# Kernel optimization log

Measured on AMD Instinct MI355X. Metric: run time of the kernel, lower is better.

The kernel has to match this reference:

```python
import jax, jax.numpy as jnp
import numpy as np

T = 1024          # tokens (flattened batch*seq)
H = 1024          # hidden_size
NH = 8            # num_attention_heads
NKV = 4           # num_key_value_heads
HD = H // NH      # head_dim = 128
E = 32            # n_routed_experts
TOPK = 4          # num_experts_per_tok
NG = 8            # n_group
TKG = 4           # topk_group
MI = 512          # moe_intermediate_size
SI = MI * 2       # shared experts intermediate (n_shared_experts=2)
THETA = 10000.0
EPS = 1e-6
RSF = 2.5         # routed_scaling_factor


def setup_inputs() -> dict:
    key = jax.random.key(0)
    ks = jax.random.split(key, 16)
    s = jnp.float32(0.02)
    def nrm(k, shape):
        return jax.random.normal(k, shape, jnp.float32) * s
    return {
        "hidden_states": jax.random.normal(ks[0], (T, H), jnp.float32),
        "position_ids": jnp.arange(T, dtype=jnp.int32),
        "ln1_w": jnp.ones((H,), jnp.float32),
        "ln2_w": jnp.ones((H,), jnp.float32),
        "q_w": nrm(ks[1], (H, H)),            # torch Linear layout [out, in]
        "k_w": nrm(ks[2], (NKV * HD, H)),
        "v_w": nrm(ks[3], (NKV * HD, H)),
        "o_w": nrm(ks[4], (H, H)),
        "router_w": nrm(ks[5], (E, H)),
        "router_bias": jnp.zeros((E,), jnp.float32),  # e_score_correction_bias
        "eg_w": nrm(ks[6], (E, H, MI)),       # expert gate_proj, [E, in, out]
        "eu_w": nrm(ks[7], (E, H, MI)),       # expert up_proj
        "ed_w": nrm(ks[8], (E, MI, H)),       # expert down_proj
        "sg_w": nrm(ks[9], (H, SI)),          # shared experts gate_proj, [in, out]
        "su_w": nrm(ks[10], (H, SI)),
        "sd_w": nrm(ks[11], (SI, H)),
    }


def rmsnorm(x, w):
    var = jnp.mean(x * x, axis=-1, keepdims=True)
    return x * jax.lax.rsqrt(var + EPS) * w


def apply_rope(x, pos):
    # x: [T, heads, HD], non-interleaved (half-rotation)
    half = HD // 2
    inv_freq = 1.0 / (THETA ** (jnp.arange(half, dtype=jnp.float32) / half))
    freqs = pos.astype(jnp.float32)[:, None] * inv_freq[None, :]  # [T, half]
    cos = jnp.cos(freqs)[:, None, :]
    sin = jnp.sin(freqs)[:, None, :]
    x1, x2 = x[..., :half], x[..., half:]
    return jnp.concatenate([x1 * cos - x2 * sin, x2 * cos + x1 * sin], axis=-1)


def attention(h, pos, q_w, k_w, v_w, o_w):
    q = (h @ q_w.T).reshape(T, NH, HD)
    k = (h @ k_w.T).reshape(T, NKV, HD)
    v = (h @ v_w.T).reshape(T, NKV, HD)
    q = apply_rope(q, pos)
    k = apply_rope(k, pos)
    rep = NH // NKV
    k = jnp.repeat(k, rep, axis=1)  # [T, NH, HD]
    v = jnp.repeat(v, rep, axis=1)
    scale = 1.0 / np.sqrt(HD).astype(np.float32)
    scores = jnp.einsum("qhd,khd->hqk", q, k) * scale  # [NH, T, T]
    causal = jnp.tril(jnp.ones((T, T), bool))
    scores = jnp.where(causal[None], scores, jnp.finfo(scores.dtype).min)
    probs = jax.nn.softmax(scores, axis=-1)
    out = jnp.einsum("hqk,khd->qhd", probs, v).reshape(T, H)
    return out @ o_w.T


def router(x, router_w, router_bias):
    logits = x.astype(jnp.float32) @ router_w.T  # [T, E]
    scores = jax.nn.sigmoid(logits)
    sfc = scores + router_bias[None, :]
    # group-limited routing: sum of top-2 per group
    group_scores = jax.lax.top_k(sfc.reshape(T, NG, E // NG), 2)[0].sum(-1)  # [T, NG]
    gidx = jax.lax.top_k(group_scores, TKG)[1]  # [T, TKG]
    gmask = jnp.zeros((T, NG), jnp.float32).at[jnp.arange(T)[:, None], gidx].set(1.0)
    smask = jnp.repeat(gmask, E // NG, axis=1) > 0  # [T, E]
    masked = jnp.where(smask, sfc, 0.0)
    topk_idx = jax.lax.top_k(masked, TOPK)[1]  # [T, TOPK]
    topk_w = jnp.take_along_axis(scores, topk_idx, axis=1)
    topk_w = topk_w / (topk_w.sum(-1, keepdims=True) + 1e-20)  # norm_topk_prob
    return topk_idx, topk_w * RSF


def moe(x, router_w, router_bias, eg_w, eu_w, ed_w, sg_w, su_w, sd_w):
    topk_idx, topk_w = router(x, router_w, router_bias)
    # combine weights [T, E]
    cw = jnp.zeros((T, E), jnp.float32).at[jnp.arange(T)[:, None], topk_idx].add(topk_w)
    g = jnp.einsum("th,ehi->eti", x, eg_w)
    u = jnp.einsum("th,ehi->eti", x, eu_w)
    a = jax.nn.silu(g) * u
    o = jnp.einsum("eti,eih->eth", a, ed_w)
    routed = jnp.einsum("eth,te->th", o, cw)
    shared = (jax.nn.silu(x @ sg_w) * (x @ su_w)) @ sd_w
    return routed + shared


def reference(hidden_states, position_ids, ln1_w, ln2_w, q_w, k_w, v_w, o_w,
              router_w, router_bias, eg_w, eu_w, ed_w, sg_w, su_w, sd_w):
    res = hidden_states
    h = rmsnorm(hidden_states, ln1_w)
    h = attention(h, position_ids, q_w, k_w, v_w, o_w)
    h = res + h
    res = h
    h = rmsnorm(h, ln2_w)
    h = moe(h, router_w, router_bias, eg_w, eu_w, ed_w, sg_w, su_w, sd_w)
    return h + res
```

## Files before the change

kernel.cpp:

```cpp
#include <hip/hip_runtime.h>
#include <math.h>

#define T 1024
#define H 1024
#define NH 8
#define NKV 4
#define HD 128
#define NE 32
#define TOPK 4
#define NG 8
#define MI 512
#define SI 1024
#define RSF 2.5f
#define EPS 1e-6f

#define ASPLIT 4
#define SPLITK 256

typedef short bf16x8 __attribute__((ext_vector_type(8)));
typedef float f32x4 __attribute__((ext_vector_type(4)));
#define MFMA16(a, b, c) __builtin_amdgcn_mfma_f32_16x16x32_bf16((a), (b), (c), 0, 0, 0)

__device__ inline unsigned short f2bf(float x) {
    unsigned u = __float_as_uint(x);
    u += 0x7fff + ((u >> 16) & 1);
    return (unsigned short)(u >> 16);
}
__device__ inline float bf2f(unsigned short h) { return __uint_as_float(((unsigned)h) << 16); }

union U16S {
    unsigned short s[16];
    uint4 q[2];
};

__device__ __forceinline__ void gl16(const void* g, void* l) {
    __builtin_amdgcn_global_load_lds((const __attribute__((address_space(1))) unsigned int*)g,
                                     (__attribute__((address_space(3))) unsigned int*)l, 16, 0, 0);
}

__global__ void rmsnorm_split_kernel(const float* __restrict__ x, const float* __restrict__ w,
                                     unsigned short* __restrict__ oh,
                                     unsigned short* __restrict__ ol) {
    int t = blockIdx.x;
    __shared__ float red[256];
    const float* xr = x + (size_t)t * H;
    float s = 0.f;
    for (int i = threadIdx.x; i < H; i += 256) { float v = xr[i]; s += v * v; }
    red[threadIdx.x] = s;
    __syncthreads();
    for (int st = 128; st > 0; st >>= 1) {
        if (threadIdx.x < st) red[threadIdx.x] += red[threadIdx.x + st];
        __syncthreads();
    }
    float inv = rsqrtf(red[0] / (float)H + EPS);
    for (int i = threadIdx.x; i < H; i += 256) {
        float v = xr[i] * inv * w[i];
        unsigned short hb = f2bf(v);
        oh[(size_t)t * H + i] = hb;
        ol[(size_t)t * H + i] = f2bf(v - bf2f(hb));
    }
}

__global__ void rmsnorm_dual_kernel(const float* __restrict__ x, const float* __restrict__ w,
                                    float* __restrict__ outf, unsigned short* __restrict__ outb) {
    int t = blockIdx.x;
    __shared__ float red[256];
    const float* xr = x + (size_t)t * H;
    float s = 0.f;
    for (int i = threadIdx.x; i < H; i += 256) { float v = xr[i]; s += v * v; }
    red[threadIdx.x] = s;
    __syncthreads();
    for (int st = 128; st > 0; st >>= 1) {
        if (threadIdx.x < st) red[threadIdx.x] += red[threadIdx.x + st];
        __syncthreads();
    }
    float inv = rsqrtf(red[0] / (float)H + EPS);
    for (int i = threadIdx.x; i < H; i += 256) {
        float v = xr[i] * inv * w[i];
        outf[(size_t)t * H + i] = v;
        outb[(size_t)t * H + i] = f2bf(v);
    }
}

__global__ void split_w4(const float* __restrict__ qw, const float* __restrict__ kw,
                         const float* __restrict__ vw, const float* __restrict__ ow,
                         unsigned short* __restrict__ qh, unsigned short* __restrict__ ql,
                         unsigned short* __restrict__ kh, unsigned short* __restrict__ kl,
                         unsigned short* __restrict__ vh, unsigned short* __restrict__ vl,
                         unsigned short* __restrict__ oh, unsigned short* __restrict__ ol) {
    int z = blockIdx.z;
    const float* src;
    unsigned short *dh, *dl;
    int n;
    if (z == 0) { src = qw; dh = qh; dl = ql; n = H * H; }
    else if (z == 1) { src = kw; dh = kh; dl = kl; n = NKV * HD * H; }
    else if (z == 2) { src = vw; dh = vh; dl = vl; n = NKV * HD * H; }
    else { src = ow; dh = oh; dl = ol; n = H * H; }
    int i = (blockIdx.x * 256 + threadIdx.x) * 4;
    if (i >= n) return;
    float4 val = *(const float4*)&src[i];
    float vv[4] = {val.x, val.y, val.z, val.w};
    unsigned short hs[4], ls[4];
#pragma unroll
    for (int j = 0; j < 4; ++j) {
        hs[j] = f2bf(vv[j]);
        ls[j] = f2bf(vv[j] - bf2f(hs[j]));
    }
    uint2 hp, lp;
    hp.x = (unsigned)hs[0] | ((unsigned)hs[1] << 16);
    hp.y = (unsigned)hs[2] | ((unsigned)hs[3] << 16);
    lp.x = (unsigned)ls[0] | ((unsigned)ls[1] << 16);
    lp.y = (unsigned)ls[2] | ((unsigned)ls[3] << 16);
    *(uint2*)&dh[i] = hp;
    *(uint2*)&dl[i] = lp;
}

__global__ __launch_bounds__(256) void transpose_cvt(const float* __restrict__ W,
                                                     unsigned short* __restrict__ Wt, int K,
                                                     int N, int eoff) {
    int zl = blockIdx.z;
    const float* src = W + (size_t)(eoff + zl) * K * N;
    unsigned short* dst = Wt + (size_t)zl * K * N;
    int k0 = blockIdx.y * 64, n0 = blockIdx.x * 64;
    __shared__ unsigned short Ls[64][70];
    int tid = threadIdx.x;
    int nn = (tid & 15) * 4, kr = tid >> 4;
#pragma unroll
    for (int p = 0; p < 4; ++p) {
        int k = kr + p * 16;
        float4 v = *(const float4*)&src[(size_t)(k0 + k) * N + n0 + nn];
        Ls[k][nn] = f2bf(v.x);
        Ls[k][nn + 1] = f2bf(v.y);
        Ls[k][nn + 2] = f2bf(v.z);
        Ls[k][nn + 3] = f2bf(v.w);
    }
    __syncthreads();
    int n = tid >> 2, kq = (tid & 3) * 16;
    U16S o;
#pragma unroll
    for (int j = 0; j < 16; ++j) o.s[j] = Ls[kq + j][n];
    unsigned short* drow = dst + (size_t)(n0 + n) * K + k0 + kq;
    *(uint4*)drow = o.q[0];
    *(uint4*)(drow + 8) = o.q[1];
}

__global__ __launch_bounds__(256) void router_logits_kernel(const float* __restrict__ x,
                                                            const float* __restrict__ W,
                                                            float* __restrict__ logits) {
    int t = blockIdx.x;
    __shared__ float xs[H];
    int tid = threadIdx.x;
    *(float4*)&xs[tid * 4] = *(const float4*)&x[(size_t)t * H + tid * 4];
    __syncthreads();
    int e = tid >> 3, p = tid & 7;
    const float* wr = W + (size_t)e * H;
    float s = 0.f;
#pragma unroll
    for (int i = 0; i < 32; ++i) {
        int k = i * 32 + p * 4;
        float4 wv = *(const float4*)&wr[k];
        float4 xv = *(const float4*)&xs[k];
        s += wv.x * xv.x + wv.y * xv.y + wv.z * xv.z + wv.w * xv.w;
    }
#pragma unroll
    for (int off = 1; off < 8; off <<= 1) s += __shfl_xor(s, off);
    if (p == 0) logits[(size_t)t * NE + e] = s;
}

__global__ __launch_bounds__(256) void gemm3_qkv(
    const unsigned short* __restrict__ Xh, const unsigned short* __restrict__ Xl,
    const unsigned short* __restrict__ Wqh, const unsigned short* __restrict__ Wql,
    const unsigned short* __restrict__ Wkh, const unsigned short* __restrict__ Wkl,
    const unsigned short* __restrict__ Wvh, const unsigned short* __restrict__ Wvl,
    float* __restrict__ qo, float* __restrict__ ko, float* __restrict__ vo) {
    __shared__ short Ahs[2][128][32], Als[2][128][32], Bhs[2][64][32], Bls[2][64][32];
    int tid = threadIdx.x;
    int m0 = blockIdx.y * 128;
    int n0 = blockIdx.x * 64;
    const unsigned short *Wh, *Wl;
    float* O;
    int ldo, nc0;
    if (n0 < 1024) { nc0 = n0; Wh = Wqh; Wl = Wql; O = qo; ldo = H; }
    else if (n0 < 1536) { nc0 = n0 - 1024; Wh = Wkh; Wl = Wkl; O = ko; ldo = NKV * HD; }
    else { nc0 = n0 - 1536; Wh = Wvh; Wl = Wvl; O = vo; ldo = NKV * HD; }
    int wave = tid >> 6, lane = tid & 63;
    int lr = lane & 15, lq = lane >> 4;
    int wm = (wave >> 1) * 64, wn = (wave & 1) * 32;
    int srow = lane >> 2, skb = (lane & 3) * 8;
    const unsigned short *ah_p[2], *al_p[2];
#pragma unroll
    for (int p = 0; p < 2; ++p) {
        int m = m0 + wave * 32 + p * 16 + srow;
        ah_p[p] = Xh + (size_t)m * H + skb;
        al_p[p] = Xl + (size_t)m * H + skb;
    }
    int bn = nc0 + wave * 16 + srow;
    const unsigned short* bh_p = Wh + (size_t)bn * H + skb;
    const unsigned short* bl_p = Wl + (size_t)bn * H + skb;
    f32x4 acc[4][2];
#pragma unroll
    for (int i = 0; i < 4; ++i)
#pragma unroll
        for (int j = 0; j < 2; ++j) acc[i][j] = (f32x4){0.f, 0.f, 0.f, 0.f};
    for (int k0 = 0; k0 < H; k0 += 64) {
#pragma unroll
        for (int c = 0; c < 2; ++c) {
            int kc = k0 + c * 32;
#pragma unroll
            for (int p = 0; p < 2; ++p) {
                gl16(ah_p[p] + kc, &Ahs[c][wave * 32 + p * 16 + srow][skb]);
                gl16(al_p[p] + kc, &Als[c][wave * 32 + p * 16 + srow][skb]);
            }
            gl16(bh_p + kc, &Bhs[c][wave * 16 + srow][skb]);
            gl16(bl_p + kc, &Bls[c][wave * 16 + srow][skb]);
        }
        __syncthreads();
#pragma unroll
        for (int c = 0; c < 2; ++c) {
            bf16x8 a_h[4], a_l[4], b_h[2], b_l[2];
#pragma unroll
            for (int mt = 0; mt < 4; ++mt) {
                a_h[mt] = *(const bf16x8*)&Ahs[c][wm + mt * 16 + lr][lq * 8];
                a_l[mt] = *(const bf16x8*)&Als[c][wm + mt * 16 + lr][lq * 8];
            }
#pragma unroll
            for (int nt = 0; nt < 2; ++nt) {
                b_h[nt] = *(const bf16x8*)&Bhs[c][wn + nt * 16 + lr][lq * 8];
                b_l[nt] = *(const bf16x8*)&Bls[c][wn + nt * 16 + lr][lq * 8];
            }
#pragma unroll
            for (int mt = 0; mt < 4; ++mt)
#pragma unroll
                for (int nt = 0; nt < 2; ++nt) {
                    acc[mt][nt] = MFMA16(a_h[mt], b_h[nt], acc[mt][nt]);
                    acc[mt][nt] = MFMA16(a_h[mt], b_l[nt], acc[mt][nt]);
                    acc[mt][nt] = MFMA16(a_l[mt], b_h[nt], acc[mt][nt]);
                }
        }
        __syncthreads();
    }
#pragma unroll
    for (int mt = 0; mt < 4; ++mt)
#pragma unroll
        for (int nt = 0; nt < 2; ++nt)
#pragma unroll
            for (int p = 0; p < 4; ++p) {
                int m = m0 + wm + mt * 16 + lq * 4 + p;
                int col = nc0 + wn + nt * 16 + lr;
                O[(size_t)m * ldo + col] = acc[mt][nt][p];
            }
}

__global__ __launch_bounds__(256) void gemm3_res(
    const unsigned short* __restrict__ Agh, const unsigned short* __restrict__ Agl,
    const unsigned short* __restrict__ Wh, const unsigned short* __restrict__ Wl,
    const float* __restrict__ res, float* __restrict__ O) {
    __shared__ short Ahs[2][128][32], Als[2][128][32], Bhs[2][64][32], Bls[2][64][32];
    int tid = threadIdx.x;
    int m0 = blockIdx.y * 128;
    int n0 = blockIdx.x * 64;
    int wave = tid >> 6, lane = tid & 63;
    int lr = lane & 15, lq = lane >> 4;
    int wm = (wave >> 1) * 64, wn = (wave & 1) * 32;
    int srow = lane >> 2, skb = (lane & 3) * 8;
    const unsigned short *ah_p[2], *al_p[2];
#pragma unroll
    for (int p = 0; p < 2; ++p) {
        int m = m0 + wave * 32 + p * 16 + srow;
        ah_p[p] = Agh + (size_t)m * H + skb;
        al_p[p] = Agl + (size_t)m * H + skb;
    }
    int bn = n0 + wave * 16 + srow;
    const unsigned short* bh_p = Wh + (size_t)bn * H + skb;
    const unsigned short* bl_p = Wl + (size_t)bn * H + skb;
    f32x4 acc[4][2];
#pragma unroll
    for (int i = 0; i < 4; ++i)
#pragma unroll
        for (int j = 0; j < 2; ++j) acc[i][j] = (f32x4){0.f, 0.f, 0.f, 0.f};
    for (int k0 = 0; k0 < H; k0 += 64) {
#pragma unroll
        for (int c = 0; c < 2; ++c) {
            int kc = k0 + c * 32;
#pragma unroll
            for (int p = 0; p < 2; ++p) {
                gl16(ah_p[p] + kc, &Ahs[c][wave * 32 + p * 16 + srow][skb]);
                gl16(al_p[p] + kc, &Als[c][wave * 32 + p * 16 + srow][skb]);
            }
            gl16(bh_p + kc, &Bhs[c][wave * 16 + srow][skb]);
            gl16(bl_p + kc, &Bls[c][wave * 16 + srow][skb]);
        }
        __syncthreads();
#pragma unroll
        for (int c = 0; c < 2; ++c) {
            bf16x8 a_h[4], a_l[4], b_h[2], b_l[2];
#pragma unroll
            for (int mt = 0; mt < 4; ++mt) {
                a_h[mt] = *(const bf16x8*)&Ahs[c][wm + mt * 16 + lr][lq * 8];
                a_l[mt] = *(const bf16x8*)&Als[c][wm + mt * 16 + lr][lq * 8];
            }
#pragma unroll
            for (int nt = 0; nt < 2; ++nt) {
                b_h[nt] = *(const bf16x8*)&Bhs[c][wn + nt * 16 + lr][lq * 8];
                b_l[nt] = *(const bf16x8*)&Bls[c][wn + nt * 16 + lr][lq * 8];
            }
#pragma unroll
            for (int mt = 0; mt < 4; ++mt)
#pragma unroll
                for (int nt = 0; nt < 2; ++nt) {
                    acc[mt][nt] = MFMA16(a_h[mt], b_h[nt], acc[mt][nt]);
                    acc[mt][nt] = MFMA16(a_h[mt], b_l[nt], acc[mt][nt]);
                    acc[mt][nt] = MFMA16(a_l[mt], b_h[nt], acc[mt][nt]);
                }
        }
        __syncthreads();
    }
#pragma unroll
    for (int mt = 0; mt < 4; ++mt)
#pragma unroll
        for (int nt = 0; nt < 2; ++nt)
#pragma unroll
            for (int p = 0; p < 4; ++p) {
                int m = m0 + wm + mt * 16 + lq * 4 + p;
                int col = n0 + wn + nt * 16 + lr;
                O[(size_t)m * H + col] = res[(size_t)m * H + col] + acc[mt][nt][p];
            }
}

__global__ void rope_kernel(float* __restrict__ q, float* __restrict__ k,
                            const int* __restrict__ pos) {
    int i = blockIdx.x * 256 + threadIdx.x;
    const int totq = T * NH * 64;
    const int tot = totq + T * NKV * 64;
    if (i >= tot) return;
    float* buf;
    int t, hh, d, nh;
    if (i < totq) {
        buf = q; nh = NH;
        int r = i; d = r & 63; r >>= 6; hh = r % NH; t = r / NH;
    } else {
        buf = k; nh = NKV;
        int r = i - totq; d = r & 63; r >>= 6; hh = r % NKV; t = r / NKV;
    }
    float p = (float)pos[t];
    float inv = powf(10000.0f, -(float)d / 64.0f);
    float fr = p * inv;
    float sv, cv;
    sincosf(fr, &sv, &cv);
    size_t bi = ((size_t)t * nh + hh) * HD + d;
    float x1 = buf[bi], x2 = buf[bi + 64];
    buf[bi] = x1 * cv - x2 * sv;
    buf[bi + 64] = x2 * cv + x1 * sv;
}

#define KS_LD 140
#define VS_LD 42
#define PS_LD 34
__global__ __launch_bounds__(256) void attn_split(const float* __restrict__ Q,
                                                  const float* __restrict__ Kb,
                                                  const float* __restrict__ Vb,
                                                  float* __restrict__ po,
                                                  float* __restrict__ pm,
                                                  float* __restrict__ pl) {
    int h = blockIdx.x;
    int qb = blockIdx.y;
    int sp = blockIdx.z;
    int kvh = h >> 1;
    int q0 = qb * 64;
    int kend = q0 + 64;
    int ks = sp * SPLITK;
    if (ks >= kend) return;
    int ke = min(ks + SPLITK, kend);
    __shared__ short Ksh[32][KS_LD], Ksl[32][KS_LD];
    __shared__ short Vsh[128][VS_LD], Vsl[128][VS_LD];
    __shared__ short Ph[4][16][PS_LD], Pl[4][16][PS_LD];
    int tid = threadIdx.x;
    int wave = tid >> 6, lane = tid & 63;
    int lr = lane & 15, lq = lane >> 4;
    const float scale = 0.08838834764831845f;

    bf16x8 qh[4], ql[4];
    {
        const float* qrow = Q + (size_t)(q0 + wave * 16 + lr) * H + h * HD;
#pragma unroll
        for (int c = 0; c < 4; ++c) {
            float4 v0 = *(const float4*)(qrow + c * 32 + lq * 8);
            float4 v1 = *(const float4*)(qrow + c * 32 + lq * 8 + 4);
            float vv[8] = {v0.x, v0.y, v0.z, v0.w, v1.x, v1.y, v1.z, v1.w};
#pragma unroll
            for (int j = 0; j < 8; ++j) {
                unsigned short hb = f2bf(vv[j]);
                qh[c][j] = (short)hb;
                ql[c][j] = (short)f2bf(vv[j] - bf2f(hb));
            }
        }
    }
    f32x4 o[8];
#pragma unroll
    for (int nt = 0; nt < 8; ++nt) o[nt] = (f32x4){0.f, 0.f, 0.f, 0.f};
    float m_r[4] = {-1e30f, -1e30f, -1e30f, -1e30f};
    float l_r[4] = {0.f, 0.f, 0.f, 0.f};

    int kts = ks >> 5, kte = ke >> 5;
    int ntw = ((q0 + wave * 16 + 15) >> 5) + 1;
    int d0 = (tid & 31) * 4, rb = tid >> 5;

    for (int kt = kts; kt < kte; ++kt) {
        int k0 = kt * 32;
#pragma unroll
        for (int pass = 0; pass < 4; ++pass) {
            int key = rb + pass * 8;
            float4 v = *(const float4*)&Kb[(size_t)(k0 + key) * (NKV * HD) + kvh * HD + d0];
            float vv[4] = {v.x, v.y, v.z, v.w};
            uint2 hi, lo;
            unsigned short h0 = f2bf(vv[0]), h1 = f2bf(vv[1]);
            unsigned short h2b = f2bf(vv[2]), h3 = f2bf(vv[3]);
            hi.x = (unsigned)h0 | ((unsigned)h1 << 16);
            hi.y = (unsigned)h2b | ((unsigned)h3 << 16);
            lo.x = (unsigned)f2bf(vv[0] - bf2f(h0)) | ((unsigned)f2bf(vv[1] - bf2f(h1)) << 16);
            lo.y = (unsigned)f2bf(vv[2] - bf2f(h2b)) | ((unsigned)f2bf(vv[3] - bf2f(h3)) << 16);
            *(uint2*)&Ksh[key][d0] = hi;
            *(uint2*)&Ksl[key][d0] = lo;
        }
#pragma unroll
        for (int pass = 0; pass < 4; ++pass) {
            int key = rb + pass * 8;
            float4 v = *(const float4*)&Vb[(size_t)(k0 + key) * (NKV * HD) + kvh * HD + d0];
            float vv[4] = {v.x, v.y, v.z, v.w};
#pragma unroll
            for (int j = 0; j < 4; ++j) {
                unsigned short hb = f2bf(vv[j]);
                Vsh[d0 + j][key] = (short)hb;
                Vsl[d0 + j][key] = (short)f2bf(vv[j] - bf2f(hb));
            }
        }
        __syncthreads();
        if (kt < ntw) {
            f32x4 s[2];
            s[0] = (f32x4){0.f, 0.f, 0.f, 0.f};
            s[1] = (f32x4){0.f, 0.f, 0.f, 0.f};
#pragma unroll
            for (int nt = 0; nt < 2; ++nt)
#pragma unroll
                for (int c = 0; c < 4; ++c) {
                    bf16x8 kh = *(const bf16x8*)&Ksh[nt * 16 + lr][c * 32 + lq * 8];
                    bf16x8 kl = *(const bf16x8*)&Ksl[nt * 16 + lr][c * 32 + lq * 8];
                    s[nt] = MFMA16(qh[c], kh, s[nt]);
                    s[nt] = MFMA16(ql[c], kh, s[nt]);
                    s[nt] = MFMA16(qh[c], kl, s[nt]);
                }
            int gr_base = q0 + wave * 16 + lq * 4;
#pragma unroll
            for (int nt = 0; nt < 2; ++nt) {
                int gc = k0 + nt * 16 + lr;
#pragma unroll
                for (int p = 0; p < 4; ++p) {
                    float sv = s[nt][p] * scale;
                    if (gc > gr_base + p) sv = -1e30f;
                    s[nt][p] = sv;
                }
            }
            float alpha[4];
#pragma unroll
            for (int p = 0; p < 4; ++p) {
                float mx = fmaxf(s[0][p], s[1][p]);
#pragma unroll
                for (int off = 1; off < 16; off <<= 1) mx = fmaxf(mx, __shfl_xor(mx, off));
                float mn = fmaxf(m_r[p], mx);
                alpha[p] = __expf(m_r[p] - mn);
                float p0 = __expf(s[0][p] - mn);
                float p1 = __expf(s[1][p] - mn);
                float ps = p0 + p1;
#pragma unroll
                for (int off = 1; off < 16; off <<= 1) ps += __shfl_xor(ps, off);
                l_r[p] = l_r[p] * alpha[p] + ps;
                m_r[p] = mn;
                int r = lq * 4 + p;
                unsigned short h0 = f2bf(p0);
                Ph[wave][r][lr] = (short)h0;
                Pl[wave][r][lr] = (short)f2bf(p0 - bf2f(h0));
                unsigned short h1 = f2bf(p1);
                Ph[wave][r][lr + 16] = (short)h1;
                Pl[wave][r][lr + 16] = (short)f2bf(p1 - bf2f(h1));
            }
            bf16x8 pah = *(const bf16x8*)&Ph[wave][lr][lq * 8];
            bf16x8 pal = *(const bf16x8*)&Pl[wave][lr][lq * 8];
#pragma unroll
            for (int nt = 0; nt < 8; ++nt) {
#pragma unroll
                for (int p = 0; p < 4; ++p) o[nt][p] *= alpha[p];
                bf16x8 vh = *(const bf16x8*)&Vsh[nt * 16 + lr][lq * 8];
                bf16x8 vl = *(const bf16x8*)&Vsl[nt * 16 + lr][lq * 8];
                o[nt] = MFMA16(pah, vh, o[nt]);
                o[nt] = MFMA16(pal, vh, o[nt]);
                o[nt] = MFMA16(pah, vl, o[nt]);
            }
        }
        __syncthreads();
    }
    int pbase = (h * 16 + qb) * ASPLIT + sp;
    float* porow = po + (size_t)pbase * (64 * 128);
#pragma unroll
    for (int nt = 0; nt < 8; ++nt)
#pragma unroll
        for (int p = 0; p < 4; ++p) {
            int row = wave * 16 + lq * 4 + p;
            porow[row * 128 + nt * 16 + lr] = o[nt][p];
        }
    if (lr == 0) {
#pragma unroll
        for (int p = 0; p < 4; ++p) {
            int row = wave * 16 + lq * 4 + p;
            pm[(size_t)pbase * 64 + row] = m_r[p];
            pl[(size_t)pbase * 64 + row] = l_r[p];
        }
    }
}

__global__ __launch_bounds__(256) void attn_merge(const float* __restrict__ po,
                                                  const float* __restrict__ pm,
                                                  const float* __restrict__ pl,
                                                  unsigned short* __restrict__ Oh,
                                                  unsigned short* __restrict__ Ol) {
    int h = blockIdx.x, qb = blockIdx.y;
    int nact = qb / 4 + 1;
    int tid = threadIdx.x;
    int row = tid >> 2;
    int c0 = (tid & 3) * 32;
    int pb = (h * 16 + qb) * ASPLIT;
    float ms[ASPLIT], ws[ASPLIT];
    float mstar = -1e30f;
    for (int s = 0; s < nact; ++s) {
        ms[s] = pm[(size_t)(pb + s) * 64 + row];
        mstar = fmaxf(mstar, ms[s]);
    }
    float lstar = 0.f;
    for (int s = 0; s < nact; ++s) {
        ws[s] = __expf(ms[s] - mstar);
        lstar += ws[s] * pl[(size_t)(pb + s) * 64 + row];
    }
    float linv = 1.f / lstar;
    size_t obase = (size_t)(qb * 64 + row) * H + h * HD + c0;
#pragma unroll
    for (int j = 0; j < 32; j += 4) {
        float acc[4] = {0.f, 0.f, 0.f, 0.f};
        for (int s = 0; s < nact; ++s) {
            float4 v = *(const float4*)&po[(size_t)(pb + s) * (64 * 128) + row * 128 + c0 + j];
            acc[0] += ws[s] * v.x;
            acc[1] += ws[s] * v.y;
            acc[2] += ws[s] * v.z;
            acc[3] += ws[s] * v.w;
        }
#pragma unroll
        for (int q = 0; q < 4; ++q) {
            float v = acc[q] * linv;
            unsigned short hb = f2bf(v);
            Oh[obase + j + q] = hb;
            Ol[obase + j + q] = f2bf(v - bf2f(hb));
        }
    }
}

__global__ void router_kernel(const float* __restrict__ logits, const float* __restrict__ bias,
                              int* __restrict__ topk_idx, float* __restrict__ topkw) {
    int t = blockIdx.x * 256 + threadIdx.x;
    if (t >= T) return;
    float sc[NE], sfc[NE];
    for (int e = 0; e < NE; ++e) {
        float s = 1.f / (1.f + expf(-logits[(size_t)t * NE + e]));
        sc[e] = s;
        sfc[e] = s + bias[e];
    }
    float gs[NG];
    for (int g = 0; g < NG; ++g) {
        float m1 = -1e30f, m2 = -1e30f;
        for (int i = 0; i < 4; ++i) {
            float v = sfc[g * 4 + i];
            if (v > m1) { m2 = m1; m1 = v; }
            else if (v > m2) m2 = v;
        }
        gs[g] = m1 + m2;
    }
    bool gmask[NG];
    for (int g = 0; g < NG; ++g) gmask[g] = false;
    for (int r = 0; r < 4; ++r) {
        int bi = 0; float bv = -1e30f;
        for (int g = 0; g < NG; ++g)
            if (gs[g] > bv) { bv = gs[g]; bi = g; }
        gmask[bi] = true;
        gs[bi] = -1e30f;
    }
    float msfc[NE];
    for (int e = 0; e < NE; ++e) msfc[e] = gmask[e >> 2] ? sfc[e] : 0.f;
    int idx[TOPK]; float w[TOPK]; float wsum = 0.f;
    for (int r = 0; r < TOPK; ++r) {
        int bi = 0; float bv = -1e30f;
        for (int e = 0; e < NE; ++e)
            if (msfc[e] > bv) { bv = msfc[e]; bi = e; }
        idx[r] = bi;
        msfc[bi] = -1e30f;
        w[r] = sc[bi];
        wsum += w[r];
    }
    float inv = RSF / (wsum + 1e-20f);
    for (int r = 0; r < TOPK; ++r) {
        topk_idx[(size_t)t * TOPK + r] = idx[r];
        topkw[(size_t)t * TOPK + r] = w[r] * inv;
    }
}

__global__ void bucket_kernel(const int* __restrict__ topk_idx, int* __restrict__ counts,
                              int* __restrict__ offs, int* __restrict__ tok_of,
                              int* __restrict__ slot_of) {
    __shared__ int cnt[NE], off[NE], fil[NE];
    int tid = threadIdx.x;
    if (tid < NE) { cnt[tid] = 0; fil[tid] = 0; }
    __syncthreads();
    for (int i = tid; i < T * TOPK; i += 256) atomicAdd(&cnt[topk_idx[i]], 1);
    __syncthreads();
    if (tid == 0) {
        int a = 0;
        for (int e = 0; e < NE; ++e) { off[e] = a; a += cnt[e]; }
    }
    __syncthreads();
    if (tid < NE) { counts[tid] = cnt[tid]; offs[tid] = off[tid]; }
    for (int i = tid; i < T * TOPK; i += 256) {
        int e = topk_idx[i];
        int p = off[e] + atomicAdd(&fil[e], 1);
        tok_of[p] = i >> 2;
        slot_of[i] = p;
    }
}

__global__ __launch_bounds__(256) void up_mfma2(
    const unsigned short* __restrict__ Xb, const unsigned short* __restrict__ Gt,
    const unsigned short* __restrict__ Ut, size_t wstride, const int* __restrict__ tok_of,
    const int* __restrict__ offs, const int* __restrict__ counts, int eoff,
    unsigned short* __restrict__ outb, int ldo) {
    int zl = blockIdx.z;
    int e = eoff + zl;
    int cnt = counts ? counts[e] : T;
    int base = offs ? offs[e] : 0;
    int m0 = blockIdx.y * 128;
    if (m0 >= cnt) return;
    int n0 = blockIdx.x * 64;
    const unsigned short* gt = Gt + (size_t)zl * wstride;
    const unsigned short* ut = Ut + (size_t)zl * wstride;
    __shared__ short As[2][128][32];
    __shared__ short Gs[2][64][32];
    __shared__ short Us[2][64][32];
    __shared__ int toks[128];
    int tid = threadIdx.x;
    if (tid < 128) {
        int m = m0 + tid;
        if (m >= cnt) m = cnt - 1;
        toks[tid] = tok_of ? tok_of[base + m] : m;
    }
    __syncthreads();
    int wave = tid >> 6, lane = tid & 63;
    int lr = lane & 15, lq = lane >> 4;
    int wm = (wave >> 1) * 64, wn = (wave & 1) * 32;
    int srow = lane >> 2, skb = (lane & 3) * 8;
    const unsigned short* aptr[2];
#pragma unroll
    for (int p = 0; p < 2; ++p)
        aptr[p] = Xb + (size_t)toks[wave * 32 + p * 16 + srow] * H + skb;
    const unsigned short* gptr = gt + (size_t)(n0 + wave * 16 + srow) * H + skb;
    const unsigned short* uptr = ut + (size_t)(n0 + wave * 16 + srow) * H + skb;
    f32x4 ag[4][2], au[4][2];
#pragma unroll
    for (int i = 0; i < 4; ++i)
#pragma unroll
        for (int j = 0; j < 2; ++j) {
            ag[i][j] = (f32x4){0.f, 0.f, 0.f, 0.f};
            au[i][j] = (f32x4){0.f, 0.f, 0.f, 0.f};
        }
    for (int k0 = 0; k0 < H; k0 += 64) {
#pragma unroll
        for (int c = 0; c < 2; ++c) {
            int kc = k0 + c * 32;
#pragma unroll
            for (int p = 0; p < 2; ++p)
                gl16(aptr[p] + kc, &As[c][wave * 32 + p * 16 + srow][skb]);
            gl16(gptr + kc, &Gs[c][wave * 16 + srow][skb]);
            gl16(uptr + kc, &Us[c][wave * 16 + srow][skb]);
        }
        __syncthreads();
#pragma unroll
        for (int c = 0; c < 2; ++c) {
            bf16x8 a[4], gg[2], uu[2];
#pragma unroll
            for (int mt = 0; mt < 4; ++mt)
                a[mt] = *(const bf16x8*)&As[c][wm + mt * 16 + lr][lq * 8];
#pragma unroll
            for (int nt = 0; nt < 2; ++nt) {
                gg[nt] = *(const bf16x8*)&Gs[c][wn + nt * 16 + lr][lq * 8];
                uu[nt] = *(const bf16x8*)&Us[c][wn + nt * 16 + lr][lq * 8];
            }
#pragma unroll
            for (int mt = 0; mt < 4; ++mt)
#pragma unroll
                for (int nt = 0; nt < 2; ++nt) {
                    ag[mt][nt] = MFMA16(a[mt], gg[nt], ag[mt][nt]);
                    au[mt][nt] = MFMA16(a[mt], uu[nt], au[mt][nt]);
                }
        }
        __syncthreads();
    }
#pragma unroll
    for (int mt = 0; mt < 4; ++mt)
#pragma unroll
        for (int nt = 0; nt < 2; ++nt)
#pragma unroll
            for (int p = 0; p < 4; ++p) {
                int m = m0 + wm + mt * 16 + lq * 4 + p;
                if (m >= cnt) continue;
                int orow = tok_of ? base + m : m;
                int col = n0 + wn + nt * 16 + lr;
                float gv = ag[mt][nt][p], uv = au[mt][nt][p];
                float sv = gv / (1.f + __expf(-gv)) * uv;
                outb[(size_t)orow * ldo + col] = f2bf(sv);
            }
}

__global__ __launch_bounds__(256) void down_mfma2(const unsigned short* __restrict__ Ab, int K,
                                                  const unsigned short* __restrict__ Wt,
                                                  size_t wstride, const int* __restrict__ offs,
                                                  const int* __restrict__ counts, int eoff,
                                                  float* __restrict__ Co) {
    int zl = blockIdx.z;
    int e = eoff + zl;
    int cnt = counts ? counts[e] : T;
    int base = offs ? offs[e] : 0;
    int m0 = blockIdx.y * 128;
    if (m0 >= cnt) return;
    int n0 = blockIdx.x * 128;
    const unsigned short* wt = Wt + (size_t)zl * wstride;
    __shared__ short As[2][128][32];
    __shared__ short Bs[2][128][32];
    int tid = threadIdx.x;
    int wave = tid >> 6, lane = tid & 63;
    int lr = lane & 15, lq = lane >> 4;
    int wm = (wave >> 1) * 64, wn = (wave & 1) * 64;
    int srow = lane >> 2, skb = (lane & 3) * 8;
    const unsigned short* aptr[2];
    const unsigned short* bptr[2];
#pragma unroll
    for (int p = 0; p < 2; ++p) {
        int m = m0 + wave * 32 + p * 16 + srow;
        if (m >= cnt) m = cnt - 1;
        aptr[p] = Ab + (size_t)(base + m) * K + skb;
        bptr[p] = wt + (size_t)(n0 + wave * 32 + p * 16 + srow) * K + skb;
    }
    f32x4 acc[4][4];
#pragma unroll
    for (int i = 0; i < 4; ++i)
#pragma unroll
        for (int j = 0; j < 4; ++j) acc[i][j] = (f32x4){0.f, 0.f, 0.f, 0.f};
    for (int k0 = 0; k0 < K; k0 += 64) {
#pragma unroll
        for (int c = 0; c < 2; ++c) {
            int kc = k0 + c * 32;
#pragma unroll
            for (int p = 0; p < 2; ++p) {
                gl16(aptr[p] + kc, &As[c][wave * 32 + p * 16 + srow][skb]);
                gl16(bptr[p] + kc, &Bs[c][wave * 32 + p * 16 + srow][skb]);
            }
        }
        __syncthreads();
#pragma unroll
        for (int c = 0; c < 2; ++c) {
            bf16x8 a[4], b[4];
#pragma unroll
            for (int mt = 0; mt < 4; ++mt)
                a[mt] = *(const bf16x8*)&As[c][wm + mt * 16 + lr][lq * 8];
#pragma unroll
            for (int nt = 0; nt < 4; ++nt)
                b[nt] = *(const bf16x8*)&Bs[c][wn + nt * 16 + lr][lq * 8];
#pragma unroll
            for (int mt = 0; mt < 4; ++mt)
#pragma unroll
                for (int nt = 0; nt < 4; ++nt) acc[mt][nt] = MFMA16(a[mt], b[nt], acc[mt][nt]);
        }
        __syncthreads();
    }
#pragma unroll
    for (int mt = 0; mt < 4; ++mt)
#pragma unroll
        for (int nt = 0; nt < 4; ++nt)
#pragma unroll
            for (int p = 0; p < 4; ++p) {
                int m = m0 + wm + mt * 16 + lq * 4 + p;
                if (m >= cnt) continue;
                int col = n0 + wn + nt * 16 + lr;
                Co[(size_t)(base + m) * H + col] = acc[mt][nt][p];
            }
}

__global__ void combine_kernel(const float* __restrict__ o_slot, const int* __restrict__ slot_of,
                               const float* __restrict__ topkw, const float* __restrict__ h2,
                               const float* __restrict__ sharedo, float* __restrict__ out) {
    int t = blockIdx.x;
    int d = threadIdx.x * 4;
    float4 a = *(const float4*)&h2[(size_t)t * H + d];
    float4 b = *(const float4*)&sharedo[(size_t)t * H + d];
    float4 acc = make_float4(a.x + b.x, a.y + b.y, a.z + b.z, a.w + b.w);
#pragma unroll
    for (int r = 0; r < TOPK; ++r) {
        int s = slot_of[t * TOPK + r];
        float w = topkw[t * TOPK + r];
        float4 v = *(const float4*)&o_slot[(size_t)s * H + d];
        acc.x += w * v.x; acc.y += w * v.y; acc.z += w * v.z; acc.w += w * v.w;
    }
    *(float4*)&out[(size_t)t * H + d] = acc;
}

extern "C" void kernel_launch(void* const* d_in, const int* in_sizes, int n_in,
                              void* d_out, int out_size, void* d_ws, size_t ws_size,
                              hipStream_t stream) {
    const float* hidden = (const float*)d_in[0];
    const int* pos = (const int*)d_in[1];
    const float* ln1w = (const float*)d_in[2];
    const float* ln2w = (const float*)d_in[3];
    const float* q_w = (const float*)d_in[4];
    const float* k_w = (const float*)d_in[5];
    const float* v_w = (const float*)d_in[6];
    const float* o_w = (const float*)d_in[7];
    const float* router_w = (const float*)d_in[8];
    const float* router_b = (const float*)d_in[9];
    const float* eg_w = (const float*)d_in[10];
    const float* eu_w = (const float*)d_in[11];
    const float* ed_w = (const float*)d_in[12];
    const float* sg_w = (const float*)d_in[13];
    const float* su_w = (const float*)d_in[14];
    const float* sd_w = (const float*)d_in[15];
    float* out = (float*)d_out;

    float* f = (float*)d_ws;
    float* xslot = f;   f += (size_t)T * H;
    float* qb = f;      f += (size_t)T * H;
    float* kb = f;      f += (size_t)T * NKV * HD;
    float* vb = f;      f += (size_t)T * NKV * HD;
    float* aoslot = f;  f += (size_t)T * H;
    float* ext = f;     f += (size_t)4 * 1024 * 1024;
    float* h2 = f;      f += (size_t)T * H;
    float* h_ln2f = f;  f += (size_t)T * H;
    float* logits = f;  f += (size_t)T * NE;
    float* topkw = f;   f += (size_t)T * TOPK;
    float* o_slot = f;  f += (size_t)T * TOPK * H;
    float* sharedo = f; f += (size_t)T * H;
    unsigned short* h_ln2b = (unsigned short*)f;
    unsigned short* abuf = h_ln2b + (size_t)T * H;
    unsigned short* ashared = abuf + (size_t)T * TOPK * MI;
    int* topk_idx = (int*)(ashared + (size_t)T * SI);
    int* counts = topk_idx + T * TOPK;
    int* fills = counts + NE;
    int* offs = fills + NE;
    int* tok_of = offs + NE;
    int* slot_of = tok_of + T * TOPK;
    (void)fills;

    unsigned short* We = (unsigned short*)ext;
    const size_t HH = (size_t)H * H;
    const size_t KH = (size_t)NKV * HD * H;
    unsigned short* Wqh = We;
    unsigned short* Wql = Wqh + HH;
    unsigned short* Wkh = Wql + HH;
    unsigned short* Wkl = Wkh + KH;
    unsigned short* Wvh = Wkl + KH;
    unsigned short* Wvl = Wvh + KH;
    unsigned short* Woh = Wvl + KH;
    unsigned short* Wol = Woh + HH;

    unsigned short* Xh = (unsigned short*)xslot;
    unsigned short* Xl = Xh + (size_t)T * H;
    unsigned short* Aoh = (unsigned short*)aoslot;
    unsigned short* Aol = Aoh + (size_t)T * H;

    float* attn_po = o_slot;
    float* attn_pm = sharedo;
    float* attn_pl = sharedo + (size_t)NH * 16 * ASPLIT * 64;

    unsigned short* arena = (unsigned short*)xslot;
    unsigned short* egT = arena;
    unsigned short* euT = arena + (size_t)16 * H * MI;
    unsigned short* edT = arena;
    unsigned short* sgT = arena;
    unsigned short* suT = arena + (size_t)H * SI;
    unsigned short* sdT = arena;

    dim3 b256(256);

    split_w4<<<dim3(HH / (256 * 4), 1, 4), b256, 0, stream>>>(q_w, k_w, v_w, o_w, Wqh, Wql,
                                                              Wkh, Wkl, Wvh, Wvl, Woh, Wol);
    rmsnorm_split_kernel<<<T, b256, 0, stream>>>(hidden, ln1w, Xh, Xl);

    gemm3_qkv<<<dim3(32, 8), b256, 0, stream>>>(Xh, Xl, Wqh, Wql, Wkh, Wkl, Wvh, Wvl,
                                                qb, kb, vb);
    {
        int tot = T * NH * 64 + T * NKV * 64;
        rope_kernel<<<(tot + 255) / 256, b256, 0, stream>>>(qb, kb, pos);
    }
    attn_split<<<dim3(NH, T / 64, ASPLIT), b256, 0, stream>>>(qb, kb, vb, attn_po, attn_pm,
                                                              attn_pl);
    attn_merge<<<dim3(NH, T / 64), b256, 0, stream>>>(attn_po, attn_pm, attn_pl, Aoh, Aol);
    gemm3_res<<<dim3(16, 8), b256, 0, stream>>>(Aoh, Aol, Woh, Wol, hidden, h2);
    rmsnorm_dual_kernel<<<T, b256, 0, stream>>>(h2, ln2w, h_ln2f, h_ln2b);

    router_logits_kernel<<<T, b256, 0, stream>>>(h_ln2f, router_w, logits);
    router_kernel<<<(T + 255) / 256, b256, 0, stream>>>(logits, router_b, topk_idx, topkw);
    bucket_kernel<<<1, b256, 0, stream>>>(topk_idx, counts, offs, tok_of, slot_of);

    for (int g = 0; g < 2; ++g) {
        int eo = g * 16;
        transpose_cvt<<<dim3(MI / 64, H / 64, 16), b256, 0, stream>>>(eg_w, egT, H, MI, eo);
        transpose_cvt<<<dim3(MI / 64, H / 64, 16), b256, 0, stream>>>(eu_w, euT, H, MI, eo);
        up_mfma2<<<dim3(MI / 64, 8, 16), b256, 0, stream>>>(
            h_ln2b, egT, euT, (size_t)H * MI, tok_of, offs, counts, eo, abuf, MI);
    }
    for (int g = 0; g < 2; ++g) {
        int eo = g * 16;
        transpose_cvt<<<dim3(H / 64, MI / 64, 16), b256, 0, stream>>>(ed_w, edT, MI, H, eo);
        down_mfma2<<<dim3(H / 128, 8, 16), b256, 0, stream>>>(
            abuf, MI, edT, (size_t)MI * H, offs, counts, eo, o_slot);
    }
    transpose_cvt<<<dim3(SI / 64, H / 64, 1), b256, 0, stream>>>(sg_w, sgT, H, SI, 0);
    transpose_cvt<<<dim3(SI / 64, H / 64, 1), b256, 0, stream>>>(su_w, suT, H, SI, 0);
    up_mfma2<<<dim3(SI / 64, T / 128, 1), b256, 0, stream>>>(
        h_ln2b, sgT, suT, 0, nullptr, nullptr, nullptr, 0, ashared, SI);
    transpose_cvt<<<dim3(H / 64, SI / 64, 1), b256, 0, stream>>>(sd_w, sdT, SI, H, 0);
    down_mfma2<<<dim3(H / 128, T / 128, 1), b256, 0, stream>>>(
        ashared, SI, sdT, 0, nullptr, nullptr, 0, sharedo);

    combine_kernel<<<T, b256, 0, stream>>>(o_slot, slot_of, topkw, h2, sharedo, out);
}
```

Baseline: 574.1 us.

## Precompute bf16 hi/lo K and transposed V, prefetch tiles, finer attention split

RoPE now writes K directly as bf16 hi/lo pairs, and a new vt_split kernel writes V transposed as bf16 hi/lo. The attention kernel therefore loads pre-split data with 16-byte loads and register-prefetches the next tile while computing the current one, instead of converting fp32 to bf16 in its inner loop. The KV split doubles, and partial results are compacted by causal slot count so only active splits get storage. The cost is an extra kernel launch plus extra global traffic for the pre-split K/V buffers, and scratch buffers are reassigned to other slots.

New measurement: 581.2 us. About the same (+1.2%).

```diff
diff --git a/kernel.cpp b/kernel.cpp
--- a/kernel.cpp
+++ b/kernel.cpp
@@ -14,8 +14,9 @@
 #define RSF 2.5f
 #define EPS 1e-6f
 
-#define ASPLIT 4
-#define SPLITK 256
+#define ASPLIT 8
+#define SPLITK 128
+#define NPSLOT 72
 
 typedef short bf16x8 __attribute__((ext_vector_type(8)));
 typedef float f32x4 __attribute__((ext_vector_type(4)));
@@ -27,6 +28,11 @@
     return (unsigned short)(u >> 16);
 }
 __device__ inline float bf2f(unsigned short h) { return __uint_as_float(((unsigned)h) << 16); }
+
+__device__ __host__ inline int cqb_of(int qb) {
+    int a = qb >> 1;
+    return (qb & 1) ? (a + 1) * (a + 1) : a * (a + 1);
+}
 
 union U16S {
     unsigned short s[16];
@@ -142,6 +148,40 @@
     unsigned short* drow = dst + (size_t)(n0 + n) * K + k0 + kq;
     *(uint4*)drow = o.q[0];
     *(uint4*)(drow + 8) = o.q[1];
+}
+
+__global__ __launch_bounds__(256) void vt_split(const float* __restrict__ vb,
+                                                unsigned short* __restrict__ VTh,
+                                                unsigned short* __restrict__ VTl) {
+    int t0 = blockIdx.x * 64, c0 = blockIdx.y * 64;
+    __shared__ unsigned short Hs[64][70], Lsh[64][70];
+    int tid = threadIdx.x;
+    int nn = (tid & 15) * 4, kr = tid >> 4;
+#pragma unroll
+    for (int p = 0; p < 4; ++p) {
+        int t = kr + p * 16;
+        float4 v = *(const float4*)&vb[(size_t)(t0 + t) * (NKV * HD) + c0 + nn];
+        float vv[4] = {v.x, v.y, v.z, v.w};
+#pragma unroll
+        for (int j = 0; j < 4; ++j) {
+            unsigned short hb = f2bf(vv[j]);
+            Hs[t][nn + j] = hb;
+            Lsh[t][nn + j] = f2bf(vv[j] - bf2f(hb));
+        }
+    }
+    __syncthreads();
+    int n = tid >> 2, kq = (tid & 3) * 16;
+    U16S oh, ol;
+#pragma unroll
+    for (int j = 0; j < 16; ++j) {
+        oh.s[j] = Hs[kq + j][n];
+        ol.s[j] = Lsh[kq + j][n];
+    }
+    size_t drow = (size_t)(c0 + n) * T + t0 + kq;
+    *(uint4*)&VTh[drow] = oh.q[0];
+    *(uint4*)&VTh[drow + 8] = oh.q[1];
+    *(uint4*)&VTl[drow] = ol.q[0];
+    *(uint4*)&VTl[drow + 8] = ol.q[1];
 }
 
 __global__ __launch_bounds__(256) void router_logits_kernel(const float* __restrict__ x,
@@ -327,38 +367,55 @@
             }
 }
 
-__global__ void rope_kernel(float* __restrict__ q, float* __restrict__ k,
-                            const int* __restrict__ pos) {
+__global__ void rope_kernel(float* __restrict__ q, const float* __restrict__ k,
+                            const int* __restrict__ pos, unsigned short* __restrict__ Khg,
+                            unsigned short* __restrict__ Klg) {
     int i = blockIdx.x * 256 + threadIdx.x;
     const int totq = T * NH * 64;
     const int tot = totq + T * NKV * 64;
     if (i >= tot) return;
-    float* buf;
-    int t, hh, d, nh;
     if (i < totq) {
-        buf = q; nh = NH;
-        int r = i; d = r & 63; r >>= 6; hh = r % NH; t = r / NH;
+        int r = i;
+        int d = r & 63; r >>= 6;
+        int hh = r % NH, t = r / NH;
+        float p = (float)pos[t];
+        float inv = powf(10000.0f, -(float)d / 64.0f);
+        float fr = p * inv;
+        float sv, cv;
+        sincosf(fr, &sv, &cv);
+        size_t bi = ((size_t)t * NH + hh) * HD + d;
+        float x1 = q[bi], x2 = q[bi + 64];
+        q[bi] = x1 * cv - x2 * sv;
+        q[bi + 64] = x2 * cv + x1 * sv;
     } else {
-        buf = k; nh = NKV;
-        int r = i - totq; d = r & 63; r >>= 6; hh = r % NKV; t = r / NKV;
-    }
-    float p = (float)pos[t];
-    float inv = powf(10000.0f, -(float)d / 64.0f);
-    float fr = p * inv;
-    float sv, cv;
-    sincosf(fr, &sv, &cv);
-    size_t bi = ((size_t)t * nh + hh) * HD + d;
-    float x1 = buf[bi], x2 = buf[bi + 64];
-    buf[bi] = x1 * cv - x2 * sv;
-    buf[bi + 64] = x2 * cv + x1 * sv;
-}
-
-#define KS_LD 140
-#define VS_LD 42
+        int r = i - totq;
+        int d = r & 63; r >>= 6;
+        int hh = r % NKV, t = r / NKV;
+        float p = (float)pos[t];
+        float inv = powf(10000.0f, -(float)d / 64.0f);
+        float fr = p * inv;
+        float sv, cv;
+        sincosf(fr, &sv, &cv);
+        size_t bi = ((size_t)t * NKV + hh) * HD + d;
+        float x1 = k[bi], x2 = k[bi + 64];
+        float n1 = x1 * cv - x2 * sv;
+        float n2 = x2 * cv + x1 * sv;
+        unsigned short h1 = f2bf(n1), h2b = f2bf(n2);
+        Khg[bi] = h1;
+        Khg[bi + 64] = h2b;
+        Klg[bi] = f2bf(n1 - bf2f(h1));
+        Klg[bi + 64] = f2bf(n2 - bf2f(h2b));
+    }
+}
+
+#define KS_LD 136
+#define VS_LD 40
 #define PS_LD 34
 __global__ __launch_bounds__(256) void attn_split(const float* __restrict__ Q,
-                                                  const float* __restrict__ Kb,
-                                                  const float* __restrict__ Vb,
+                                                  const unsigned short* __restrict__ Khg,
+                                                  const unsigned short* __restrict__ Klg,
+                                                  const unsigned short* __restrict__ VTh,
+                                                  const unsigned short* __restrict__ VTl,
                                                   float* __restrict__ po,
                                                   float* __restrict__ pm,
                                                   float* __restrict__ pl) {
@@ -371,8 +428,8 @@
     int ks = sp * SPLITK;
     if (ks >= kend) return;
     int ke = min(ks + SPLITK, kend);
-    __shared__ short Ksh[32][KS_LD], Ksl[32][KS_LD];
-    __shared__ short Vsh[128][VS_LD], Vsl[128][VS_LD];
+    __shared__ __attribute__((aligned(16))) short Ksh[32][KS_LD], Ksl[32][KS_LD];
+    __shared__ __attribute__((aligned(16))) short Vsh[128][VS_LD], Vsl[128][VS_LD];
     __shared__ short Ph[4][16][PS_LD], Pl[4][16][PS_LD];
     int tid = threadIdx.x;
     int wave = tid >> 6, lane = tid & 63;
@@ -403,38 +460,43 @@
 
     int kts = ks >> 5, kte = ke >> 5;
     int ntw = ((q0 + wave * 16 + 15) >> 5) + 1;
-    int d0 = (tid & 31) * 4, rb = tid >> 5;
-
+
+    int key_k = tid >> 3, kc = (tid & 7) * 16;
+    int d_v = tid >> 1, vc = (tid & 1) * 16;
+    const unsigned short* kbase_h = Khg + (size_t)kvh * HD + kc;
+    const unsigned short* kbase_l = Klg + (size_t)kvh * HD + kc;
+    const unsigned short* vbase_h = VTh + (size_t)(kvh * HD + d_v) * T + vc;
+    const unsigned short* vbase_l = VTl + (size_t)(kvh * HD + d_v) * T + vc;
+
+    uint4 kr0, kr1, kr2, kr3, vr0, vr1, vr2, vr3;
+#define LOADT(KT)                                                                    \
+    {                                                                                \
+        size_t koff = (size_t)((KT)*32 + key_k) * (NKV * HD);                        \
+        kr0 = *(const uint4*)(kbase_h + koff);                                       \
+        kr1 = *(const uint4*)(kbase_h + koff + 8);                                   \
+        kr2 = *(const uint4*)(kbase_l + koff);                                       \
+        kr3 = *(const uint4*)(kbase_l + koff + 8);                                   \
+        int voff = (KT)*32;                                                          \
+        vr0 = *(const uint4*)(vbase_h + voff);                                       \
+        vr1 = *(const uint4*)(vbase_h + voff + 8);                                   \
+        vr2 = *(const uint4*)(vbase_l + voff);                                       \
+        vr3 = *(const uint4*)(vbase_l + voff + 8);                                   \
+    }
+
+    LOADT(kts);
     for (int kt = kts; kt < kte; ++kt) {
         int k0 = kt * 32;
-#pragma unroll
-        for (int pass = 0; pass < 4; ++pass) {
-            int key = rb + pass * 8;
-            float4 v = *(const float4*)&Kb[(size_t)(k0 + key) * (NKV * HD) + kvh * HD + d0];
-            float vv[4] = {v.x, v.y, v.z, v.w};
-            uint2 hi, lo;
-            unsigned short h0 = f2bf(vv[0]), h1 = f2bf(vv[1]);
-            unsigned short h2b = f2bf(vv[2]), h3 = f2bf(vv[3]);
-            hi.x = (unsigned)h0 | ((unsigned)h1 << 16);
-            hi.y = (unsigned)h2b | ((unsigned)h3 << 16);
-            lo.x = (unsigned)f2bf(vv[0] - bf2f(h0)) | ((unsigned)f2bf(vv[1] - bf2f(h1)) << 16);
-            lo.y = (unsigned)f2bf(vv[2] - bf2f(h2b)) | ((unsigned)f2bf(vv[3] - bf2f(h3)) << 16);
-            *(uint2*)&Ksh[key][d0] = hi;
-            *(uint2*)&Ksl[key][d0] = lo;
-        }
-#pragma unroll
-        for (int pass = 0; pass < 4; ++pass) {
-            int key = rb + pass * 8;
-            float4 v = *(const float4*)&Vb[(size_t)(k0 + key) * (NKV * HD) + kvh * HD + d0];
-            float vv[4] = {v.x, v.y, v.z, v.w};
-#pragma unroll
-            for (int j = 0; j < 4; ++j) {
-                unsigned short hb = f2bf(vv[j]);
-                Vsh[d0 + j][key] = (short)hb;
-                Vsl[d0 + j][key] = (short)f2bf(vv[j] - bf2f(hb));
-            }
-        }
-        __syncthreads();
+        __syncthreads();
+        *(uint4*)&Ksh[key_k][kc] = kr0;
+        *(uint4*)&Ksh[key_k][kc + 8] = kr1;
+        *(uint4*)&Ksl[key_k][kc] = kr2;
+        *(uint4*)&Ksl[key_k][kc + 8] = kr3;
+        *(uint4*)&Vsh[d_v][vc] = vr0;
+        *(uint4*)&Vsh[d_v][vc + 8] = vr1;
+        *(uint4*)&Vsl[d_v][vc] = vr2;
+        *(uint4*)&Vsl[d_v][vc + 8] = vr3;
+        __syncthreads();
+        if (kt + 1 < kte) LOADT(kt + 1);
         if (kt < ntw) {
             f32x4 s[2];
             s[0] = (f32x4){0.f, 0.f, 0.f, 0.f};
@@ -496,9 +558,9 @@
                 o[nt] = MFMA16(pah, vl, o[nt]);
             }
         }
-        __syncthreads();
-    }
-    int pbase = (h * 16 + qb) * ASPLIT + sp;
+    }
+#undef LOADT
+    int pbase = h * NPSLOT + cqb_of(qb) + sp;
     float* porow = po + (size_t)pbase * (64 * 128);
 #pragma unroll
     for (int nt = 0; nt < 8; ++nt)
@@ -523,34 +585,41 @@
                                                   unsigned short* __restrict__ Oh,
                                                   unsigned short* __restrict__ Ol) {
     int h = blockIdx.x, qb = blockIdx.y;
-    int nact = qb / 4 + 1;
+    int nact = qb / 2 + 1;
     int tid = threadIdx.x;
     int row = tid >> 2;
     int c0 = (tid & 3) * 32;
-    int pb = (h * 16 + qb) * ASPLIT;
+    int pb = h * NPSLOT + cqb_of(qb);
     float ms[ASPLIT], ws[ASPLIT];
     float mstar = -1e30f;
-    for (int s = 0; s < nact; ++s) {
-        ms[s] = pm[(size_t)(pb + s) * 64 + row];
-        mstar = fmaxf(mstar, ms[s]);
-    }
+#pragma unroll
+    for (int s = 0; s < ASPLIT; ++s)
+        if (s < nact) {
+            ms[s] = pm[(size_t)(pb + s) * 64 + row];
+            mstar = fmaxf(mstar, ms[s]);
+        }
     float lstar = 0.f;
-    for (int s = 0; s < nact; ++s) {
-        ws[s] = __expf(ms[s] - mstar);
-        lstar += ws[s] * pl[(size_t)(pb + s) * 64 + row];
-    }
+#pragma unroll
+    for (int s = 0; s < ASPLIT; ++s)
+        if (s < nact) {
+            ws[s] = __expf(ms[s] - mstar);
+            lstar += ws[s] * pl[(size_t)(pb + s) * 64 + row];
+        }
     float linv = 1.f / lstar;
     size_t obase = (size_t)(qb * 64 + row) * H + h * HD + c0;
 #pragma unroll
     for (int j = 0; j < 32; j += 4) {
         float acc[4] = {0.f, 0.f, 0.f, 0.f};
-        for (int s = 0; s < nact; ++s) {
-            float4 v = *(const float4*)&po[(size_t)(pb + s) * (64 * 128) + row * 128 + c0 + j];
-            acc[0] += ws[s] * v.x;
-            acc[1] += ws[s] * v.y;
-            acc[2] += ws[s] * v.z;
-            acc[3] += ws[s] * v.w;
-        }
+#pragma unroll
+        for (int s = 0; s < ASPLIT; ++s)
+            if (s < nact) {
+                float4 v =
+                    *(const float4*)&po[(size_t)(pb + s) * (64 * 128) + row * 128 + c0 + j];
+                acc[0] += ws[s] * v.x;
+                acc[1] += ws[s] * v.y;
+                acc[2] += ws[s] * v.z;
+                acc[3] += ws[s] * v.w;
+            }
 #pragma unroll
         for (int q = 0; q < 4; ++q) {
             float v = acc[q] * linv;
@@ -877,9 +946,14 @@
     unsigned short* Aoh = (unsigned short*)aoslot;
     unsigned short* Aol = Aoh + (size_t)T * H;
 
+    unsigned short* Khg = (unsigned short*)xslot;
+    unsigned short* Klg = Khg + (size_t)T * NKV * HD;
+    unsigned short* VTh = Klg + (size_t)T * NKV * HD;
+    unsigned short* VTl = VTh + (size_t)T * NKV * HD;
+
     float* attn_po = o_slot;
-    float* attn_pm = sharedo;
-    float* attn_pl = sharedo + (size_t)NH * 16 * ASPLIT * 64;
+    float* attn_pm = (float*)abuf;
+    float* attn_pl = attn_pm + (size_t)NH * NPSLOT * 64;
 
     unsigned short* arena = (unsigned short*)xslot;
     unsigned short* egT = arena;
@@ -899,10 +973,11 @@
                                                 qb, kb, vb);
     {
         int tot = T * NH * 64 + T * NKV * 64;
-        rope_kernel<<<(tot + 255) / 256, b256, 0, stream>>>(qb, kb, pos);
-    }
-    attn_split<<<dim3(NH, T / 64, ASPLIT), b256, 0, stream>>>(qb, kb, vb, attn_po, attn_pm,
-                                                              attn_pl);
+        rope_kernel<<<(tot + 255) / 256, b256, 0, stream>>>(qb, kb, pos, Khg, Klg);
+    }
+    vt_split<<<dim3(T / 64, (NKV * HD) / 64), b256, 0, stream>>>(vb, VTh, VTl);
+    attn_split<<<dim3(NH, T / 64, ASPLIT), b256, 0, stream>>>(qb, Khg, Klg, VTh, VTl,
+                                                              attn_po, attn_pm, attn_pl);
     attn_merge<<<dim3(NH, T / 64), b256, 0, stream>>>(attn_po, attn_pm, attn_pl, Aoh, Aol);
     gemm3_res<<<dim3(16, 8), b256, 0, stream>>>(Aoh, Aol, Woh, Wol, hidden, h2);
     rmsnorm_dual_kernel<<<T, b256, 0, stream>>>(h2, ln2w, h_ln2f, h_ln2b);
```
